# Kernel tuning notes

Hardware: AMD Instinct MI355X
Metric: run time of the kernel (lower is better)

## Reference

```python
import jax, jax.numpy as jnp
import numpy as np

HEAD_DIM = 64

def rotate_half(x):
    x1, x2 = jnp.split(x, 2, axis=-1)
    return jnp.concatenate([-x2, x1], axis=-1)

def setup_inputs() -> dict:
    key = jax.random.key(0)
    ks = jax.random.split(key, 6)
    B, T, E = 1, 2048, 2048
    H, KV, D = 32, 8, HEAD_DIM
    BS, W = 64, 256
    hidden_states = jax.random.normal(ks[0], (B, T, E), jnp.float32)
    Wq = jax.random.normal(ks[1], (H * D, E), jnp.float32) / np.float32(np.sqrt(E))
    Wk = jax.random.normal(ks[2], (KV * D, E), jnp.float32) / np.float32(np.sqrt(E))
    Wv = jax.random.normal(ks[3], (KV * D, E), jnp.float32) / np.float32(np.sqrt(E))
    Wo = jax.random.normal(ks[4], (E, H * D), jnp.float32) / np.float32(np.sqrt(H * D))
    # RoPE tables (Llama-style, theta=10000)
    pos = jnp.arange(T, dtype=jnp.float32)
    inv_freq = 1.0 / (10000.0 ** (jnp.arange(0, D, 2, dtype=jnp.float32) / D))
    freqs = pos[:, None] * inv_freq[None, :]                 # [T, D/2]
    emb = jnp.concatenate([freqs, freqs], axis=-1)           # [T, D]
    cos = jnp.cos(emb)[None]                                 # [1, T, D]
    sin = jnp.sin(emb)[None]
    rw_allow_blocks = jax.random.bernoulli(ks[5], 0.15, (B, T // BS, T // BS))
    return {"hidden_states": hidden_states, "cos": cos, "sin": sin,
            "Wq": Wq, "Wk": Wk, "Wv": Wv, "Wo": Wo,
            "rw_allow_blocks": rw_allow_blocks,
            "rw_block_size": BS, "rw_window_tokens": W}

def reference(hidden_states, cos, sin, Wq, Wk, Wv, Wo,
              rw_allow_blocks, rw_block_size, rw_window_tokens):
    B, T, E = hidden_states.shape
    D = HEAD_DIM
    H = Wq.shape[0] // D
    KV = Wk.shape[0] // D
    n_rep = H // KV  # num_key_value_groups
    scaling = D ** -0.5

    # projections -> [B, heads, T, D]
    q = (hidden_states @ Wq.T).reshape(B, T, H, D).transpose(0, 2, 1, 3)
    k = (hidden_states @ Wk.T).reshape(B, T, KV, D).transpose(0, 2, 1, 3)
    v = (hidden_states @ Wv.T).reshape(B, T, KV, D).transpose(0, 2, 1, 3)

    # rotary embedding (unsqueeze_dim=1)
    c = cos[:, None, :, :]
    s = sin[:, None, :, :]
    q = q * c + rotate_half(q) * s
    k = k * c + rotate_half(k) * s

    # repeat_kv for GQA
    k = jnp.repeat(k, n_rep, axis=1)
    v = jnp.repeat(v, n_rep, axis=1)

    scores = jnp.einsum('bhqd,bhkd->bhqk', q, k) * scaling   # [B,H,T,T]

    # expand block allow pattern to token resolution
    allow = jnp.repeat(jnp.repeat(rw_allow_blocks, rw_block_size, axis=1),
                       rw_block_size, axis=2)[:, :T, :T]     # [B,T,T]
    # causal sliding window + attention sink (first window tokens always visible)
    qi = jnp.arange(T)[:, None]
    ki = jnp.arange(T)[None, :]
    win = ((ki <= qi) & (ki >= qi - rw_window_tokens + 1)) | (ki < rw_window_tokens)
    allow = allow | win[None]

    neg = jnp.finfo(scores.dtype).min
    scores = jnp.where(allow[:, None, :, :], scores, neg)
    probs = jax.nn.softmax(scores.astype(jnp.float32), axis=-1).astype(q.dtype)

    out = jnp.einsum('bhqk,bhkd->bhqd', probs, v)            # [B,H,T,D]
    out = out.transpose(0, 2, 1, 3).reshape(B, T, H * D)
    return out @ Wo.T                                        # [B,T,E]
```

## Files before the change

kernel.cpp:

```cpp
#include <hip/hip_runtime.h>

typedef unsigned short bfu;
typedef __attribute__((ext_vector_type(8))) short short8;
typedef __attribute__((ext_vector_type(4))) float f32x4;

#define TT 2048
#define EE 2048

#define GBAR() do { __builtin_amdgcn_sched_barrier(0); \
                    __builtin_amdgcn_s_barrier();      \
                    __builtin_amdgcn_sched_barrier(0); } while (0)

__device__ __forceinline__ unsigned short f2bf(float f) {
  union { float fv; unsigned int u; } v; v.fv = f;
  unsigned int r = v.u + 0x7fffu + ((v.u >> 16) & 1u);
  return (unsigned short)(r >> 16);
}

__device__ __forceinline__ unsigned int cvtpk(float lo, float hi) {
  unsigned int r;
  asm("v_cvt_pk_bf16_f32 %0, %1, %2" : "=v"(r) : "v"(lo), "v"(hi));
  return r;
}

__device__ __forceinline__ float fexp2(float x) {
  float r;
  asm("v_exp_f32 %0, %1" : "=v"(r) : "v"(x));
  return r;
}

__device__ __forceinline__ void gload16(const void* g, void* l) {
  __builtin_amdgcn_global_load_lds(
      (const __attribute__((address_space(1))) unsigned int*)g,
      (__attribute__((address_space(3))) unsigned int*)l, 16, 0, 0);
}

__global__ __launch_bounds__(256) void cvt5(
    const float* __restrict__ s0, const float* __restrict__ s1,
    const float* __restrict__ s2, const float* __restrict__ s3,
    const float* __restrict__ s4,
    bfu* __restrict__ d0, bfu* __restrict__ d1, bfu* __restrict__ d2,
    bfu* __restrict__ d3, bfu* __restrict__ d4,
    const unsigned char* __restrict__ mask_in, unsigned char* __restrict__ mask_out) {
  if (blockIdx.y == 5) {
    if (blockIdx.x != 0) return;
    __shared__ int mis;
    if (threadIdx.x == 0) mis = 0;
    __syncthreads();
    int any = 0;
    for (int i = threadIdx.x; i < 1024; i += 256)
      if ((i & 3) != 0 && mask_in[i] != 0) any = 1;
    if (any) atomicAdd(&mis, 1);
    __syncthreads();
    for (int i = threadIdx.x; i < 1024; i += 256) {
      if (mis == 0) mask_out[i] = (((const int*)mask_in)[i] != 0) ? 1 : 0;
      else          mask_out[i] = mask_in[i] ? 1 : 0;
    }
    return;
  }
  const float* s; bfu* d; int n;
  switch (blockIdx.y) {
    case 0:  s = s0; d = d0; n = 4194304; break;
    case 1:  s = s1; d = d1; n = 4194304; break;
    case 2:  s = s2; d = d2; n = 1048576; break;
    case 3:  s = s3; d = d3; n = 1048576; break;
    default: s = s4; d = d4; n = 4194304; break;
  }
  for (int i = (blockIdx.x * 256 + threadIdx.x) * 8; i < n; i += 512 * 256 * 8) {
    float4 a = *(const float4*)(s + i);
    float4 b = *(const float4*)(s + i + 4);
    short8 pk;
    pk[0] = (short)f2bf(a.x); pk[1] = (short)f2bf(a.y);
    pk[2] = (short)f2bf(a.z); pk[3] = (short)f2bf(a.w);
    pk[4] = (short)f2bf(b.x); pk[5] = (short)f2bf(b.y);
    pk[6] = (short)f2bf(b.z); pk[7] = (short)f2bf(b.w);
    *(short8*)(d + i) = pk;
  }
}

__global__ __launch_bounds__(512) void gemm_qkv(
    const bfu* __restrict__ A, const bfu* __restrict__ Bq,
    const bfu* __restrict__ Bk, const bfu* __restrict__ Bv,
    bfu* __restrict__ qr, bfu* __restrict__ kro, bfu* __restrict__ vt,
    const float* __restrict__ cosb, const float* __restrict__ sinb, float qsc) {
  __shared__ bfu As[2][64 * 64];
  __shared__ bfu Bs[2][128 * 64];
  const int bx = blockIdx.x;
  int path, n0;
  const bfu* B;
  if (bx < 16)      { path = 0; B = Bq; n0 = bx * 128; }
  else if (bx < 20) { path = 1; B = Bk; n0 = (bx - 16) * 128; }
  else              { path = 2; B = Bv; n0 = (bx - 20) * 128; }
  const int t = threadIdx.x;
  const int wid = t >> 6, lane = t & 63;
  const int wr = wid >> 1, wc = wid & 1;
  const int lr = lane & 15, lh = lane >> 4;
  const int m0 = blockIdx.y * 64;
  const int K = EE;
  f32x4 acc[4] = {};

  const int srow = t >> 3, sslot = t & 7;
  const int browB = (t + 512) >> 3, sslotB = (t + 512) & 7;
  auto stage = [&](int buf, int k0) {
    gload16(A + (size_t)(m0 + srow) * K + k0 + ((sslot ^ (srow & 7)) * 8),
            &As[buf][wid * 512]);
    gload16(B + (size_t)(n0 + srow) * K + k0 + ((sslot ^ (srow & 7)) * 8),
            &Bs[buf][wid * 512]);
    gload16(B + (size_t)(n0 + browB) * K + k0 + ((sslotB ^ (browB & 7)) * 8),
            &Bs[buf][4096 + wid * 512]);
  };

  stage(0, 0);
  for (int kt = 0; kt < 32; ++kt) {
    const int cur = kt & 1;
    if (kt < 31) {
      stage(cur ^ 1, (kt + 1) * 64);
      asm volatile("s_waitcnt vmcnt(3)" ::: "memory");
    } else {
      asm volatile("s_waitcnt vmcnt(0)" ::: "memory");
    }
    GBAR();
    #pragma unroll
    for (int ks = 0; ks < 2; ++ks) {
      short8 a, b[4];
      a = *(const short8*)(&As[cur][(wr * 16 + lr) * 64 +
                                    (((ks * 4 + lh) ^ (lr & 7)) * 8)]);
      #pragma unroll
      for (int n = 0; n < 4; ++n)
        b[n] = *(const short8*)(&Bs[cur][(wc * 64 + n * 16 + lr) * 64 +
                                         (((ks * 4 + lh) ^ (lr & 7)) * 8)]);
      #pragma unroll
      for (int n = 0; n < 4; ++n)
        acc[n] = __builtin_amdgcn_mfma_f32_16x16x32_bf16(a, b[n], acc[n], 0, 0, 0);
    }
    GBAR();
  }
  #pragma unroll
  for (int r = 0; r < 4; ++r) {
    const int row = m0 + wr * 16 + lh * 4 + r;
    #pragma unroll
    for (int n = 0; n < 4; ++n) {
      const int col = n0 + wc * 64 + n * 16 + lr;
      float x = acc[n][r];
      if (path == 2) {
        vt[((size_t)(row >> 6) * 512 + col) * 64 + (row & 63)] = f2bf(x);
      } else {
        const int d = col & 63;
        float xp = (n < 2) ? -acc[n + 2][r] : acc[n - 2][r];
        float c = cosb[row * 64 + d], s = sinb[row * 64 + d];
        float sc = (path == 0) ? qsc : 1.0f;
        bfu* dst = (path == 0) ? qr : kro;
        dst[((size_t)(col >> 6) * TT + row) * 64 + d] = f2bf((x * c + xp * s) * sc);
      }
    }
  }
}

__global__ __launch_bounds__(512) void gemm_o(
    const bfu* __restrict__ A, const bfu* __restrict__ B,
    float* __restrict__ outF, int M, int N, int K) {
  __shared__ bfu As[2][64 * 64];
  __shared__ bfu Bs[2][128 * 64];
  const int t = threadIdx.x;
  const int wid = t >> 6, lane = t & 63;
  const int wr = wid >> 1, wc = wid & 1;
  const int lr = lane & 15, lh = lane >> 4;
  const int m0 = blockIdx.y * 64, n0 = blockIdx.x * 128;
  f32x4 acc[4] = {};

  const int srow = t >> 3, sslot = t & 7;
  const int browB = (t + 512) >> 3, sslotB = (t + 512) & 7;
  auto stage = [&](int buf, int k0) {
    gload16(A + (size_t)(m0 + srow) * K + k0 + ((sslot ^ (srow & 7)) * 8),
            &As[buf][wid * 512]);
    gload16(B + (size_t)(n0 + srow) * K + k0 + ((sslot ^ (srow & 7)) * 8),
            &Bs[buf][wid * 512]);
    gload16(B + (size_t)(n0 + browB) * K + k0 + ((sslotB ^ (browB & 7)) * 8),
            &Bs[buf][4096 + wid * 512]);
  };

  stage(0, 0);
  const int nk = K >> 6;
  for (int kt = 0; kt < nk; ++kt) {
    const int cur = kt & 1;
    if (kt < nk - 1) {
      stage(cur ^ 1, (kt + 1) * 64);
      asm volatile("s_waitcnt vmcnt(3)" ::: "memory");
    } else {
      asm volatile("s_waitcnt vmcnt(0)" ::: "memory");
    }
    GBAR();
    #pragma unroll
    for (int ks = 0; ks < 2; ++ks) {
      short8 a, b[4];
      a = *(const short8*)(&As[cur][(wr * 16 + lr) * 64 +
                                    (((ks * 4 + lh) ^ (lr & 7)) * 8)]);
      #pragma unroll
      for (int n = 0; n < 4; ++n)
        b[n] = *(const short8*)(&Bs[cur][(wc * 64 + n * 16 + lr) * 64 +
                                         (((ks * 4 + lh) ^ (lr & 7)) * 8)]);
      #pragma unroll
      for (int n = 0; n < 4; ++n)
        acc[n] = __builtin_amdgcn_mfma_f32_16x16x32_bf16(a, b[n], acc[n], 0, 0, 0);
    }
    GBAR();
  }
  #pragma unroll
  for (int r = 0; r < 4; ++r) {
    const int row = m0 + wr * 16 + lh * 4 + r;
    #pragma unroll
    for (int n = 0; n < 4; ++n)
      outF[(size_t)row * N + n0 + wc * 64 + n * 16 + lr] = acc[n][r];
  }
}

__global__ __launch_bounds__(256, 6) void attn_kernel(
    const bfu* __restrict__ qr, const bfu* __restrict__ kr,
    const bfu* __restrict__ vt, const unsigned char* __restrict__ allow,
    bfu* __restrict__ ao) {
  const int qb = blockIdx.x, h = blockIdx.y, kv = h >> 2;
  const int t = threadIdx.x, wid = t >> 6, lane = t & 63;
  const int lr = lane & 15, lh = lane >> 4;
  const int q0 = qb * 64;
  const int qrow = q0 + wid * 16 + lr;
  __shared__ bfu KB[64 * 64];
  __shared__ bfu VB[64 * 64];
  __shared__ bfu P[4][16 * 64];
  bfu* Pw = P[wid];

  unsigned int amask = 0, emask = 0;
  for (int kb = 0; kb < 32; ++kb) {
    bool bm = allow[qb * 32 + kb] != 0;
    bool fw = (kb < 4) || (kb >= qb - 3 && kb <= qb - 1);
    bool ed = (kb == qb) || (kb == qb - 4);
    if (bm || fw || ed) {
      amask |= 1u << kb;
      if (!bm && !fw) emask |= 1u << kb;
    }
  }

  short8 bq[2];
  #pragma unroll
  for (int ks = 0; ks < 2; ++ks)
    bq[ks] = *(const short8*)(qr + ((size_t)h * TT + qrow) * 64 + ks * 32 + lh * 8);

  short8 vones;
  #pragma unroll
  for (int i = 0; i < 8; ++i) vones[i] = (short)0x3F80;

  f32x4 o[4] = {};
  f32x4 o_l = {};
  float m_reg = -1e30f;

  auto stage = [&](bfu* buf, const bfu* gbase) {
    #pragma unroll
    for (int c = 0; c < 2; ++c) {
      int chunk = wid * 128 + c * 64 + lane;
      int row = chunk >> 3, s = chunk & 7;
      gload16(gbase + row * 64 + (s ^ (row & 7)) * 8,
              buf + (wid * 128 + c * 64) * 8);
    }
  };

  auto qk_tile = [&](const bfu* KBuf, int kb, f32x4 s[4]) {
    __builtin_amdgcn_s_setprio(1);
    #pragma unroll
    for (int j = 0; j < 4; ++j) {
      const int row = j * 16 + lr;
      short8 a0 = *(const short8*)(KBuf + row * 64 + ((lh    ) ^ (row & 7)) * 8);
      short8 a1 = *(const short8*)(KBuf + row * 64 + ((lh + 4) ^ (row & 7)) * 8);
      f32x4 z = {};
      z = __builtin_amdgcn_mfma_f32_16x16x32_bf16(a0, bq[0], z, 0, 0, 0);
      s[j] = __builtin_amdgcn_mfma_f32_16x16x32_bf16(a1, bq[1], z, 0, 0, 0);
    }
    __builtin_amdgcn_s_setprio(0);
    if ((emask >> kb) & 1) {
      #pragma unroll
      for (int j = 0; j < 4; ++j)
        #pragma unroll
        for (int reg = 0; reg < 4; ++reg) {
          int k = kb * 64 + j * 16 + lh * 4 + reg;
          bool ok = (k <= qrow && k >= qrow - 255) || (k < 256);
          if (!ok) s[j][reg] = -1e30f;
        }
    }
  };

  auto pv_tile = [&](const bfu* VBuf, f32x4 s[4]) {
    #pragma unroll
    for (int j = 0; j < 4; ++j) {
      unsigned int w0 = cvtpk(s[j][0], s[j][1]);
      unsigned int w1 = cvtpk(s[j][2], s[j][3]);
      int base = lr * 64 + (((j * 2 + (lh >> 1)) ^ (lr & 7)) * 8) + (lh & 1) * 4;
      *(unsigned int*)(Pw + base) = w0;
      *(unsigned int*)(Pw + base + 2) = w1;
    }
    short8 pa[2];
    #pragma unroll
    for (int ks = 0; ks < 2; ++ks)
      pa[ks] = *(const short8*)(Pw + lr * 64 + (((ks * 4 + lh) ^ (lr & 7)) * 8));
    __builtin_amdgcn_s_setprio(1);
    #pragma unroll
    for (int n = 0; n < 4; ++n) {
      #pragma unroll
      for (int ks = 0; ks < 2; ++ks) {
        const int row = n * 16 + lr;
        short8 bv = *(const short8*)(VBuf + row * 64 + ((ks * 4 + lh) ^ (row & 7)) * 8);
        o[n] = __builtin_amdgcn_mfma_f32_16x16x32_bf16(pa[ks], bv, o[n], 0, 0, 0);
      }
    }
    o_l = __builtin_amdgcn_mfma_f32_16x16x32_bf16(pa[0], vones, o_l, 0, 0, 0);
    o_l = __builtin_amdgcn_mfma_f32_16x16x32_bf16(pa[1], vones, o_l, 0, 0, 0);
    __builtin_amdgcn_s_setprio(0);
  };

  unsigned int am = amask;
  while (am) {
    const int k1 = __ffs(am) - 1; am &= am - 1;

    __syncthreads();
    stage(KB, kr + ((size_t)kv * TT + k1 * 64) * 64);
    stage(VB, vt + ((size_t)k1 * 512 + kv * 64) * 64);
    __syncthreads();

    f32x4 s1[4];
    qk_tile(KB, k1, s1);

    float mx = fmaxf(fmaxf(s1[0][0], s1[0][1]), fmaxf(s1[0][2], s1[0][3]));
    #pragma unroll
    for (int j = 1; j < 4; ++j)
      mx = fmaxf(mx, fmaxf(fmaxf(s1[j][0], s1[j][1]), fmaxf(s1[j][2], s1[j][3])));
    mx = fmaxf(mx, __shfl_xor(mx, 16));
    mx = fmaxf(mx, __shfl_xor(mx, 32));

    if (__any(mx > m_reg)) {
      float mnew = fmaxf(m_reg, mx);
      float corr = fexp2(m_reg - mnew);
      m_reg = mnew;
      #pragma unroll
      for (int r = 0; r < 4; ++r) {
        float cr = __shfl(corr, lh * 4 + r);
        #pragma unroll
        for (int n = 0; n < 4; ++n) o[n][r] *= cr;
        o_l[r] *= cr;
      }
    }

    #pragma unroll
    for (int j = 0; j < 4; ++j)
      #pragma unroll
      for (int reg = 0; reg < 4; ++reg)
        s1[j][reg] = fexp2(s1[j][reg] - m_reg);

    pv_tile(VB, s1);
  }

  #pragma unroll
  for (int r = 0; r < 4; ++r) {
    float inv = 1.0f / o_l[r];
    #pragma unroll
    for (int n = 0; n < 4; ++n) {
      float val = o[n][r] * inv;
      ao[(size_t)(q0 + wid * 16 + lh * 4 + r) * EE + h * 64 + n * 16 + lr] = f2bf(val);
    }
  }
}

extern "C" void kernel_launch(void* const* d_in, const int* in_sizes, int n_in,
                              void* d_out, int out_size, void* d_ws, size_t ws_size,
                              hipStream_t stream) {
  const float* hs   = (const float*)d_in[0];
  const float* cosb = (const float*)d_in[1];
  const float* sinb = (const float*)d_in[2];
  const float* Wq   = (const float*)d_in[3];
  const float* Wk   = (const float*)d_in[4];
  const float* Wv   = (const float*)d_in[5];
  const float* Wo   = (const float*)d_in[6];
  const unsigned char* allow_raw = (const unsigned char*)d_in[7];
  float* out = (float*)d_out;

  char* ws = (char*)d_ws;
  const size_t MB = 1024 * 1024;
  bfu* hsb = (bfu*)(ws);
  bfu* wqb = (bfu*)(ws + 8 * MB);
  bfu* wkb = (bfu*)(ws + 16 * MB);
  bfu* wvb = (bfu*)(ws + 18 * MB);
  bfu* wob = (bfu*)(ws + 20 * MB);
  bfu* qr  = (bfu*)(ws + 28 * MB);
  bfu* kr  = (bfu*)(ws + 36 * MB);
  bfu* vt  = (bfu*)(ws + 38 * MB);
  unsigned char* maskc = (unsigned char*)(ws + 40 * MB);
  bfu* ao = hsb;

  cvt5<<<dim3(512, 6), 256, 0, stream>>>(hs, Wq, Wk, Wv, Wo,
                                         hsb, wqb, wkb, wvb, wob,
                                         allow_raw, maskc);

  const float QSC = 0.125f * 1.44269504088896f;
  gemm_qkv<<<dim3(24, 32), 512, 0, stream>>>(
      hsb, wqb, wkb, wvb, qr, kr, vt, cosb, sinb, QSC);

  attn_kernel<<<dim3(32, 32), 256, 0, stream>>>(qr, kr, vt, maskc, ao);

  gemm_o<<<dim3(16, 32), 512, 0, stream>>>(ao, wob, out, 2048, 2048, 2048);
}
```

Measured before the change: 125.5 us.

## Load K/V fragments directly from global into registers, dropping LDS staging

```diff
diff --git a/kernel.cpp b/kernel.cpp
--- a/kernel.cpp
+++ b/kernel.cpp
@@ -214,7 +214,7 @@
   }
 }
 
-__global__ __launch_bounds__(256, 6) void attn_kernel(
+__global__ __launch_bounds__(256, 4) void attn_kernel(
     const bfu* __restrict__ qr, const bfu* __restrict__ kr,
     const bfu* __restrict__ vt, const unsigned char* __restrict__ allow,
     bfu* __restrict__ ao) {
@@ -223,8 +223,6 @@
   const int lr = lane & 15, lh = lane >> 4;
   const int q0 = qb * 64;
   const int qrow = q0 + wid * 16 + lr;
-  __shared__ bfu KB[64 * 64];
-  __shared__ bfu VB[64 * 64];
   __shared__ bfu P[4][16 * 64];
   bfu* Pw = P[wid];
 
@@ -252,79 +250,46 @@
   f32x4 o_l = {};
   float m_reg = -1e30f;
 
-  auto stage = [&](bfu* buf, const bfu* gbase) {
-    #pragma unroll
-    for (int c = 0; c < 2; ++c) {
-      int chunk = wid * 128 + c * 64 + lane;
-      int row = chunk >> 3, s = chunk & 7;
-      gload16(gbase + row * 64 + (s ^ (row & 7)) * 8,
-              buf + (wid * 128 + c * 64) * 8);
-    }
-  };
-
-  auto qk_tile = [&](const bfu* KBuf, int kb, f32x4 s[4]) {
-    __builtin_amdgcn_s_setprio(1);
+  unsigned int am = amask;
+  while (am) {
+    const int k1 = __ffs(am) - 1; am &= am - 1;
+    const bfu* kt_ = kr + ((size_t)kv * TT + k1 * 64) * 64;
+    const bfu* vt_ = vt + ((size_t)k1 * 512 + kv * 64) * 64;
+
+    short8 kf[8], vf[8];
     #pragma unroll
     for (int j = 0; j < 4; ++j) {
       const int row = j * 16 + lr;
-      short8 a0 = *(const short8*)(KBuf + row * 64 + ((lh    ) ^ (row & 7)) * 8);
-      short8 a1 = *(const short8*)(KBuf + row * 64 + ((lh + 4) ^ (row & 7)) * 8);
+      kf[2 * j]     = *(const short8*)(kt_ + row * 64 + lh * 8);
+      kf[2 * j + 1] = *(const short8*)(kt_ + row * 64 + 32 + lh * 8);
+    }
+    #pragma unroll
+    for (int n = 0; n < 4; ++n) {
+      const int row = n * 16 + lr;
+      vf[2 * n]     = *(const short8*)(vt_ + row * 64 + lh * 8);
+      vf[2 * n + 1] = *(const short8*)(vt_ + row * 64 + 32 + lh * 8);
+    }
+
+    f32x4 s1[4];
+    __builtin_amdgcn_s_setprio(1);
+    #pragma unroll
+    for (int j = 0; j < 4; ++j) {
       f32x4 z = {};
-      z = __builtin_amdgcn_mfma_f32_16x16x32_bf16(a0, bq[0], z, 0, 0, 0);
-      s[j] = __builtin_amdgcn_mfma_f32_16x16x32_bf16(a1, bq[1], z, 0, 0, 0);
+      z = __builtin_amdgcn_mfma_f32_16x16x32_bf16(kf[2 * j], bq[0], z, 0, 0, 0);
+      s1[j] = __builtin_amdgcn_mfma_f32_16x16x32_bf16(kf[2 * j + 1], bq[1], z, 0, 0, 0);
     }
     __builtin_amdgcn_s_setprio(0);
-    if ((emask >> kb) & 1) {
+
+    if ((emask >> k1) & 1) {
       #pragma unroll
       for (int j = 0; j < 4; ++j)
         #pragma unroll
         for (int reg = 0; reg < 4; ++reg) {
-          int k = kb * 64 + j * 16 + lh * 4 + reg;
+          int k = k1 * 64 + j * 16 + lh * 4 + reg;
           bool ok = (k <= qrow && k >= qrow - 255) || (k < 256);
-          if (!ok) s[j][reg] = -1e30f;
+          if (!ok) s1[j][reg] = -1e30f;
         }
     }
-  };
-
-  auto pv_tile = [&](const bfu* VBuf, f32x4 s[4]) {
-    #pragma unroll
-    for (int j = 0; j < 4; ++j) {
-      unsigned int w0 = cvtpk(s[j][0], s[j][1]);
-      unsigned int w1 = cvtpk(s[j][2], s[j][3]);
-      int base = lr * 64 + (((j * 2 + (lh >> 1)) ^ (lr & 7)) * 8) + (lh & 1) * 4;
-      *(unsigned int*)(Pw + base) = w0;
-      *(unsigned int*)(Pw + base + 2) = w1;
-    }
-    short8 pa[2];
-    #pragma unroll
-    for (int ks = 0; ks < 2; ++ks)
-      pa[ks] = *(const short8*)(Pw + lr * 64 + (((ks * 4 + lh) ^ (lr & 7)) * 8));
-    __builtin_amdgcn_s_setprio(1);
-    #pragma unroll
-    for (int n = 0; n < 4; ++n) {
-      #pragma unroll
-      for (int ks = 0; ks < 2; ++ks) {
-        const int row = n * 16 + lr;
-        short8 bv = *(const short8*)(VBuf + row * 64 + ((ks * 4 + lh) ^ (row & 7)) * 8);
-        o[n] = __builtin_amdgcn_mfma_f32_16x16x32_bf16(pa[ks], bv, o[n], 0, 0, 0);
-      }
-    }
-    o_l = __builtin_amdgcn_mfma_f32_16x16x32_bf16(pa[0], vones, o_l, 0, 0, 0);
-    o_l = __builtin_amdgcn_mfma_f32_16x16x32_bf16(pa[1], vones, o_l, 0, 0, 0);
-    __builtin_amdgcn_s_setprio(0);
-  };
-
-  unsigned int am = amask;
-  while (am) {
-    const int k1 = __ffs(am) - 1; am &= am - 1;
-
-    __syncthreads();
-    stage(KB, kr + ((size_t)kv * TT + k1 * 64) * 64);
-    stage(VB, vt + ((size_t)k1 * 512 + kv * 64) * 64);
-    __syncthreads();
-
-    f32x4 s1[4];
-    qk_tile(KB, k1, s1);
 
     float mx = fmaxf(fmaxf(s1[0][0], s1[0][1]), fmaxf(s1[0][2], s1[0][3]));
     #pragma unroll
@@ -352,7 +317,29 @@
       for (int reg = 0; reg < 4; ++reg)
         s1[j][reg] = fexp2(s1[j][reg] - m_reg);
 
-    pv_tile(VB, s1);
+    #pragma unroll
+    for (int j = 0; j < 4; ++j) {
+      unsigned int w0 = cvtpk(s1[j][0], s1[j][1]);
+      unsigned int w1 = cvtpk(s1[j][2], s1[j][3]);
+      int base = lr * 64 + (((j * 2 + (lh >> 1)) ^ (lr & 7)) * 8) + (lh & 1) * 4;
+      *(unsigned int*)(Pw + base) = w0;
+      *(unsigned int*)(Pw + base + 2) = w1;
+    }
+    short8 pa[2];
+    #pragma unroll
+    for (int ks = 0; ks < 2; ++ks)
+      pa[ks] = *(const short8*)(Pw + lr * 64 + (((ks * 4 + lh) ^ (lr & 7)) * 8));
+
+    __builtin_amdgcn_s_setprio(1);
+    #pragma unroll
+    for (int n = 0; n < 4; ++n) {
+      #pragma unroll
+      for (int ks = 0; ks < 2; ++ks)
+        o[n] = __builtin_amdgcn_mfma_f32_16x16x32_bf16(pa[ks], vf[2 * n + ks], o[n], 0, 0, 0);
+    }
+    o_l = __builtin_amdgcn_mfma_f32_16x16x32_bf16(pa[0], vones, o_l, 0, 0, 0);
+    o_l = __builtin_amdgcn_mfma_f32_16x16x32_bf16(pa[1], vones, o_l, 0, 0, 0);
+    __builtin_amdgcn_s_setprio(0);
   }
 
   #pragma unroll
```

Measured after the change: 207.2 us. 1.65x slower.
